# Kernel tuning notes

Measured on AMD Instinct MI355X. Metric: run time of the kernel, lower is better.

Reference implementation:

```python
import jax, jax.numpy as jnp
import numpy as np

HIDDEN = 256
BATCH = 8
N_A = 2048
N_B = 2048


def setup_inputs() -> dict:
    key = jax.random.key(0)
    ks = jax.random.split(key, 9)
    s = 1.0 / np.sqrt(HIDDEN)  # torch Linear default init scale
    return {
        "A": jax.random.normal(ks[0], (BATCH, N_A, HIDDEN), dtype=jnp.float32),
        "B": jax.random.normal(ks[1], (BATCH, N_B, HIDDEN), dtype=jnp.float32),
        "mask_B": jax.random.randint(ks[2], (BATCH, N_B), 0, 2, dtype=jnp.int32),
        "Wq": jax.random.uniform(ks[3], (HIDDEN, HIDDEN), jnp.float32, -s, s),
        "bq": jax.random.uniform(ks[4], (HIDDEN,), jnp.float32, -s, s),
        "Wk": jax.random.uniform(ks[5], (HIDDEN, HIDDEN), jnp.float32, -s, s),
        "bk": jax.random.uniform(ks[6], (HIDDEN,), jnp.float32, -s, s),
        "Wv": jax.random.uniform(ks[7], (HIDDEN, HIDDEN), jnp.float32, -s, s),
        "bv": jax.random.uniform(ks[8], (HIDDEN,), jnp.float32, -s, s),
    }


def reference(A, B, mask_B, Wq, bq, Wk, bk, Wv, bv):
    # QKV projections (torch Linear: x @ W.T + b)
    Q = A @ Wq.T + bq          # [B, N_A, H]
    K = B @ Wk.T + bk          # [B, N_B, H]
    V = B @ Wv.T + bv          # [B, N_B, H]
    scale = 1.0 / jnp.sqrt(jnp.asarray(Q.shape[-1], Q.dtype))
    scores = jnp.einsum("bnh,bmh->bnm", Q, K) * scale  # [B, N_A, N_B]
    neg_inf = jnp.finfo(scores.dtype).min
    scores = jnp.where(mask_B[:, None, :] == 0, neg_inf, scores)
    attn = jax.nn.softmax(scores, axis=-1)
    out = jnp.einsum("bnm,bmh->bnh", attn, V)          # [B, N_A, H]
    return out
```

## Files before the change

### kernel.cpp

```cpp
#include <hip/hip_runtime.h>


typedef __attribute__((ext_vector_type(8))) __bf16 bf16x8;
typedef __attribute__((ext_vector_type(4))) __bf16 bf16x4;
typedef __attribute__((ext_vector_type(4))) float f32x4;

#if __has_builtin(__builtin_amdgcn_exp2f)
#define EXP2(x) __builtin_amdgcn_exp2f(x)
#else
#define EXP2(x) exp2f(x)
#endif

#define MFMA16(a, b, c) __builtin_amdgcn_mfma_f32_16x16x32_bf16((a), (b), (c), 0, 0, 0)

typedef const __attribute__((address_space(1))) char gas_char;
typedef __attribute__((address_space(3))) char las_char;

static __device__ __forceinline__ void gload16(const void* g, void* l) {
  __builtin_amdgcn_global_load_lds((gas_char*)g, (las_char*)l, 16, 0, 0);
}

static __device__ __forceinline__ bf16x8 pack8(f32x4 a, f32x4 b) {
  bf16x8 r;
  r[0] = (__bf16)a[0]; r[1] = (__bf16)a[1]; r[2] = (__bf16)a[2]; r[3] = (__bf16)a[3];
  r[4] = (__bf16)b[0]; r[5] = (__bf16)b[1]; r[6] = (__bf16)b[2]; r[7] = (__bf16)b[3];
  return r;
}

__global__ void mask_kernel(const int* __restrict__ mask, float* __restrict__ mb) {
  int i = blockIdx.x * 256 + threadIdx.x;
  if (i < 8 * 2048) mb[i] = (mask[i] != 0) ? 0.0f : -1.0e30f;
}

__global__ __launch_bounds__(256, 4) void proj_kernel(
    const float* __restrict__ A, const float* __restrict__ Bm,
    const float* __restrict__ Wq, const float* __restrict__ bq,
    const float* __restrict__ Wk, const float* __restrict__ bk,
    const float* __restrict__ Wv, const float* __restrict__ bv,
    __bf16* __restrict__ QF, __bf16* __restrict__ KF, __bf16* __restrict__ VF) {
  __shared__ __bf16 Wl[256 * 64];
  const int pid = blockIdx.x;
  const int proj = pid >> 8;
  const int rb = (pid & 255) << 6;
  const float* __restrict__ X = (proj == 0) ? A : Bm;
  const float* __restrict__ W = (proj == 0) ? Wq : (proj == 1 ? Wk : Wv);
  const float* __restrict__ bias = (proj == 0) ? bq : (proj == 1 ? bk : bv);
  const int tid = threadIdx.x;
  const int w = tid >> 6, l = tid & 63, lo = l & 15, g = l >> 4;
  const int r0 = rb + w * 16;

  f32x4 acc[16];
#pragma unroll
  for (int j = 0; j < 16; ++j) acc[j] = (f32x4){0.f, 0.f, 0.f, 0.f};

  for (int qtr = 0; qtr < 4; ++qtr) {
    if (qtr) __syncthreads();
    for (int c = tid; c < 2048; c += 256) {
      int n = c >> 3;
      int k8 = (c & 7) << 3;
      const float* wp = &W[n * 256 + qtr * 64 + k8];
      f32x4 w0 = *(const f32x4*)wp;
      f32x4 w1 = *(const f32x4*)(wp + 4);
      int kx = k8 ^ ((n & 7) << 3);
      *(bf16x8*)&Wl[n * 64 + kx] = pack8(w0, w1);
    }
    __syncthreads();
#pragma unroll
    for (int ks2 = 0; ks2 < 2; ++ks2) {
      const int kg = qtr * 64 + ks2 * 32 + g * 8;
      const float* xp = &X[(r0 + lo) * 256 + kg];
      bf16x8 xf = pack8(*(const f32x4*)xp, *(const f32x4*)(xp + 4));
#pragma unroll
      for (int nt = 0; nt < 16; ++nt) {
        int n = nt * 16 + lo;
        int kchunk = (ks2 * 4 + g) ^ (n & 7);
        bf16x8 wf = *(const bf16x8*)&Wl[n * 64 + kchunk * 8];
        if (proj == 2) {
          acc[nt] = MFMA16(wf, xf, acc[nt]);
        } else {
          acc[nt] = MFMA16(xf, wf, acc[nt]);
        }
      }
    }
  }

  if (proj != 2) {
    const float cs = (proj == 0) ? 0.090168440f : 1.0f;
    __bf16* __restrict__ O = (proj == 0) ? QF : KF;
    const size_t rgbase = (size_t)(r0 >> 4) << 12;
#pragma unroll
    for (int nt = 0; nt < 16; ++nt) {
      int h = nt * 16 + lo;
      float bb = bias[h];
      size_t hpart = (size_t)((h >> 5) << 9) + (((h >> 3) & 3) << 7) + (h & 7);
#pragma unroll
      for (int r = 0; r < 4; ++r) {
        int R = r0 + g * 4 + r;
        O[rgbase + hpart + ((R & 15) << 3)] = (__bf16)((acc[nt][r] + bb) * cs);
      }
    }
  } else {
    const int bidx = r0 >> 11;
    const int nb = r0 & 2047;
    __bf16* __restrict__ Vo = VF + (size_t)bidx * 524288;
#pragma unroll
    for (int ht = 0; ht < 16; ++ht)
#pragma unroll
      for (int r = 0; r < 4; ++r) {
        int h = ht * 16 + g * 4 + r;
        int n = nb + lo;
        Vo[((size_t)(n >> 6) << 14) + ((h >> 4) << 10) + (((n >> 3) & 7) << 7) +
           ((h & 15) << 3) + (n & 7)] = (__bf16)(acc[ht][r] + bias[h]);
      }
  }
}

__global__ __launch_bounds__(256, 2) void attn_kernel(
    const __bf16* __restrict__ QF, const __bf16* __restrict__ KF,
    const __bf16* __restrict__ VF, const float* __restrict__ mb,
    __bf16* __restrict__ Opart, float* __restrict__ mpart,
    float* __restrict__ lpart, float* __restrict__ out,
    int chunk, int direct) {
  extern __shared__ char smem[];
  const int bid = blockIdx.x;
  const int b = bid & 7;
  const int rest = bid >> 3;
  const int qt = rest & 15;
  const int s = rest >> 4;
  const int tid = threadIdx.x;
  const int w = tid >> 6, l = tid & 63, lo = l & 15, g = l >> 4;
  const int q0 = qt * 128 + w * 32;
  const __bf16* __restrict__ Qb = QF + ((size_t)b * 2048 + q0) * 256;
  const __bf16* __restrict__ Kb = KF + (size_t)b * 2048 * 256;
  const __bf16* __restrict__ Vb = VF + (size_t)b * 524288;
  const float* __restrict__ mbb = mb + b * 2048;
  __bf16* Pw = (__bf16*)(smem + 65536) + w * 1280;
  float* mbl = (float*)(smem + 75776);

  bf16x8 qf[2][8];
#pragma unroll
  for (int u = 0; u < 2; ++u)
#pragma unroll
    for (int hs = 0; hs < 8; ++hs)
      qf[u][hs] = *(const bf16x8*)&Qb[u * 4096 + hs * 512 + l * 8];

  f32x4 oacc[2][16];
#pragma unroll
  for (int u = 0; u < 2; ++u)
#pragma unroll
    for (int i = 0; i < 16; ++i) oacc[u][i] = (f32x4){0.f, 0.f, 0.f, 0.f};
  float m[2] = {-3.0e28f, -3.0e28f}, lsum[2] = {0.f, 0.f};

  const int kv0 = s * chunk;
  const int niter = chunk >> 5;

  #define STAGE_K(kvb, buf)                                                   \
    {                                                                         \
      const char* gk = (const char*)(Kb + (size_t)(kvb) * 256) + w * 4096 +   \
                       l * 16;                                                \
      char* lk = smem + (buf)*16384 + w * 4096;                               \
      gload16(gk, lk);                                                        \
      gload16(gk + 1024, lk + 1024);                                          \
      gload16(gk + 2048, lk + 2048);                                          \
      gload16(gk + 3072, lk + 3072);                                          \
    }
  #define STAGE_V(kvb, buf)                                                   \
    {                                                                         \
      const char* gv = (const char*)(Vb + (((size_t)(kvb) >> 6) << 14) +      \
                                     (((kvb) >> 5) & 1) * 512) +              \
                       w * 8192 + l * 16;                                     \
      char* lv = smem + 32768 + (buf)*16384 + w * 4096;                       \
      gload16(gv, lv);                                                        \
      gload16(gv + 2048, lv + 1024);                                          \
      gload16(gv + 4096, lv + 2048);                                          \
      gload16(gv + 6144, lv + 3072);                                          \
    }

  if (!direct)
    for (int j = tid; j < chunk; j += 256) mbl[j] = mbb[kv0 + j];
  STAGE_K(kv0, 0);
  STAGE_V(kv0, 0);
  __syncthreads();

  for (int it = 0; it < niter; ++it) {
    const int kvb = kv0 + (it << 5);
    const int cur = it & 1;
    const bool pre = (it + 1 < niter);
    if (pre) STAGE_K(kvb + 32, cur ^ 1);
    const char* kbase = smem + cur * 16384;
    const char* vbase = smem + 32768 + cur * 16384;

    f32x4 sacc[2][2];
#pragma unroll
    for (int u = 0; u < 2; ++u)
#pragma unroll
      for (int t = 0; t < 2; ++t) sacc[u][t] = (f32x4){0.f, 0.f, 0.f, 0.f};
    __builtin_amdgcn_s_setprio(1);
#pragma unroll
    for (int t = 0; t < 2; ++t)
#pragma unroll
      for (int hs = 0; hs < 8; ++hs) {
        bf16x8 kf = *(const bf16x8*)(kbase + t * 8192 + hs * 1024 + l * 16);
        sacc[0][t] = MFMA16(kf, qf[0][hs], sacc[0][t]);
        sacc[1][t] = MFMA16(kf, qf[1][hs], sacc[1][t]);
      }
    __builtin_amdgcn_s_setprio(0);

    f32x4 bias4[2];
#pragma unroll
    for (int t = 0; t < 2; ++t) {
      if (direct)
        bias4[t] = *(const f32x4*)&mbb[kvb + t * 16 + g * 4];
      else
        bias4[t] = *(const f32x4*)&mbl[(it << 5) + t * 16 + g * 4];
    }
#pragma unroll
    for (int u = 0; u < 2; ++u) {
      float tmax = -3.4e38f;
#pragma unroll
      for (int t = 0; t < 2; ++t)
#pragma unroll
        for (int r = 0; r < 4; ++r) {
          sacc[u][t][r] += bias4[t][r];
          tmax = fmaxf(tmax, sacc[u][t][r]);
        }
      tmax = fmaxf(tmax, __shfl_xor(tmax, 16));
      tmax = fmaxf(tmax, __shfl_xor(tmax, 32));
      if (!__all(tmax <= m[u] + 8.0f)) {
        float mn = fmaxf(m[u], tmax);
        float f = EXP2(m[u] - mn);
        lsum[u] *= f;
#pragma unroll
        for (int i = 0; i < 16; ++i) {
          oacc[u][i][0] *= f; oacc[u][i][1] *= f;
          oacc[u][i][2] *= f; oacc[u][i][3] *= f;
        }
        m[u] = mn;
      }
#pragma unroll
      for (int t = 0; t < 2; ++t) {
        float p0 = EXP2(sacc[u][t][0] - m[u]);
        float p1 = EXP2(sacc[u][t][1] - m[u]);
        float p2 = EXP2(sacc[u][t][2] - m[u]);
        float p3 = EXP2(sacc[u][t][3] - m[u]);
        lsum[u] += (p0 + p1) + (p2 + p3);
        bf16x4 pk;
        pk[0] = (__bf16)p0; pk[1] = (__bf16)p1;
        pk[2] = (__bf16)p2; pk[3] = (__bf16)p3;
        *(bf16x4*)&Pw[u * 640 + lo * 40 + t * 16 + g * 4] = pk;
      }
    }
    bf16x8 pf[2];
#pragma unroll
    for (int u = 0; u < 2; ++u)
      pf[u] = *(const bf16x8*)&Pw[u * 640 + lo * 40 + g * 8];

    if (direct || !pre) {
      asm volatile("s_waitcnt vmcnt(0)" ::: "memory");
    } else {
      asm volatile("s_waitcnt vmcnt(4)" ::: "memory");
    }
    __builtin_amdgcn_s_barrier();
    __builtin_amdgcn_sched_barrier(0);

    if (pre) STAGE_V(kvb + 32, cur ^ 1);

    __builtin_amdgcn_s_setprio(1);
#pragma unroll
    for (int ht = 0; ht < 16; ++ht) {
      bf16x8 vf = *(const bf16x8*)(vbase + ht * 1024 + l * 16);
      oacc[0][ht] = MFMA16(vf, pf[0], oacc[0][ht]);
      oacc[1][ht] = MFMA16(vf, pf[1], oacc[1][ht]);
    }
    __builtin_amdgcn_s_setprio(0);

    if (direct || !pre) {
      asm volatile("s_waitcnt vmcnt(0)" ::: "memory");
    } else {
      asm volatile("s_waitcnt vmcnt(4)" ::: "memory");
    }
    __builtin_amdgcn_s_barrier();
    __builtin_amdgcn_sched_barrier(0);
  }

#pragma unroll
  for (int u = 0; u < 2; ++u) {
    float ls = lsum[u];
    ls += __shfl_xor(ls, 16);
    ls += __shfl_xor(ls, 32);
    const int q0u = q0 + u * 16;
    if (direct) {
      float inv = 1.0f / ls;
      float* __restrict__ Ob = out + ((size_t)b * 2048 + q0u) * 256;
#pragma unroll
      for (int ht = 0; ht < 16; ++ht) {
        f32x4 v = oacc[u][ht];
        v[0] *= inv; v[1] *= inv; v[2] *= inv; v[3] *= inv;
        *(f32x4*)&Ob[lo * 256 + ht * 16 + g * 4] = v;
      }
    } else {
      const size_t rowbase = (size_t)(s * 8 + b) * 2048 + q0u;
      __bf16* __restrict__ Ob = Opart + rowbase * 256;
#pragma unroll
      for (int ht = 0; ht < 16; ++ht) {
        f32x4 v = oacc[u][ht];
        bf16x4 pk;
        pk[0] = (__bf16)v[0]; pk[1] = (__bf16)v[1];
        pk[2] = (__bf16)v[2]; pk[3] = (__bf16)v[3];
        *(bf16x4*)&Ob[lo * 256 + ht * 16 + g * 4] = pk;
      }
      if (l < 16) {
        mpart[rowbase + lo] = m[u];
        lpart[rowbase + lo] = ls;
      }
    }
  }
}

__global__ __launch_bounds__(256) void combine_kernel(
    const __bf16* __restrict__ Opart, const float* __restrict__ mpart,
    const float* __restrict__ lpart, float* __restrict__ out, int nsplit) {
  int t = blockIdx.x * 256 + threadIdx.x;
  int row = t >> 6;
  int h4 = (t & 63) << 2;
  float M = -3.4e38f;
  for (int s = 0; s < nsplit; ++s) M = fmaxf(M, mpart[s * 16384 + row]);
  f32x4 acc = (f32x4){0.f, 0.f, 0.f, 0.f};
  float denom = 0.f;
  for (int s = 0; s < nsplit; ++s) {
    float wgt = EXP2(mpart[s * 16384 + row] - M);
    denom += wgt * lpart[s * 16384 + row];
    bf16x4 o = *(const bf16x4*)&Opart[((size_t)s * 16384 + row) * 256 + h4];
    acc[0] += wgt * (float)o[0]; acc[1] += wgt * (float)o[1];
    acc[2] += wgt * (float)o[2]; acc[3] += wgt * (float)o[3];
  }
  float inv = 1.0f / denom;
  f32x4 r;
  r[0] = acc[0] * inv; r[1] = acc[1] * inv;
  r[2] = acc[2] * inv; r[3] = acc[3] * inv;
  *(f32x4*)&out[(size_t)row * 256 + h4] = r;
}

extern "C" void kernel_launch(void* const* d_in, const int* in_sizes, int n_in,
                              void* d_out, int out_size, void* d_ws, size_t ws_size,
                              hipStream_t stream) {
  const float* A = (const float*)d_in[0];
  const float* B = (const float*)d_in[1];
  const int* mask = (const int*)d_in[2];
  const float* Wq = (const float*)d_in[3];
  const float* bq = (const float*)d_in[4];
  const float* Wk = (const float*)d_in[5];
  const float* bk = (const float*)d_in[6];
  const float* Wv = (const float*)d_in[7];
  const float* bv = (const float*)d_in[8];

  char* ws = (char*)d_ws;
  __bf16* QF = (__bf16*)(ws);
  __bf16* KF = (__bf16*)(ws + (8ull << 20));
  __bf16* VF = (__bf16*)(ws + (16ull << 20));
  float* mb = (float*)(ws + (24ull << 20));
  float* mpart = (float*)(ws + (24ull << 20) + 0x10000);
  float* lpart = (float*)(ws + (24ull << 20) + 0x60000);
  __bf16* Opart = (__bf16*)(ws + (25ull << 20));

  const size_t base = 25ull << 20;
  const size_t part = 8ull << 20;
  int S;
  if (ws_size >= base + 4 * part) S = 4;
  else if (ws_size >= base + 2 * part) S = 2;
  else if (ws_size >= base + 1 * part) S = 1;
  else S = 0;

  const int SMEM = 65536 + 4 * 1280 * 2 + 2048;
  (void)hipFuncSetAttribute((const void*)attn_kernel,
                            hipFuncAttributeMaxDynamicSharedMemorySize, SMEM);

  mask_kernel<<<64, 256, 0, stream>>>(mask, mb);
  proj_kernel<<<768, 256, 0, stream>>>(A, B, Wq, bq, Wk, bk, Wv, bv, QF, KF, VF);
  if (S == 0) {
    attn_kernel<<<128, 256, SMEM, stream>>>(QF, KF, VF, mb, nullptr, nullptr,
                                            nullptr, (float*)d_out, 2048, 1);
  } else {
    attn_kernel<<<128 * S, 256, SMEM, stream>>>(QF, KF, VF, mb, Opart, mpart,
                                                lpart, nullptr, 2048 / S, 0);
    combine_kernel<<<4096, 256, 0, stream>>>(Opart, mpart, lpart,
                                             (float*)d_out, S);
  }
}
```

Measured before the change: 102.7 us.

## Pre-convert weights to swizzled bf16 once and double-buffer them via async LDS loads

A new prep kernel converts Wq/Wk/Wv to bf16 in the swizzled LDS layout, folds the Q scale into Wq, and also builds the mask bias, replacing the separate mask kernel. The projection kernel then stages each weight quarter with global_load_lds into a double-buffered 64KB dynamic LDS region and prefetches all X fragments into registers up front. This removes the per-block fp32 weight conversion that every one of 768 blocks repeated, and overlaps weight loads with MFMA work. The cost is lower occupancy (launch bounds 2, 64KB LDS per block) and higher register pressure.

```diff
diff --git a/kernel.cpp b/kernel.cpp
--- a/kernel.cpp
+++ b/kernel.cpp
@@ -27,61 +27,102 @@
   return r;
 }
 
-__global__ void mask_kernel(const int* __restrict__ mask, float* __restrict__ mb) {
-  int i = blockIdx.x * 256 + threadIdx.x;
-  if (i < 8 * 2048) mb[i] = (mask[i] != 0) ? 0.0f : -1.0e30f;
-}
-
-__global__ __launch_bounds__(256, 4) void proj_kernel(
+__global__ __launch_bounds__(256) void wprep_kernel(
+    const float* __restrict__ Wq, const float* __restrict__ Wk,
+    const float* __restrict__ Wv, const int* __restrict__ mask,
+    __bf16* __restrict__ Wb, float* __restrict__ mb) {
+  const int bid = blockIdx.x;
+  if (bid < 96) {
+    int c = bid * 256 + threadIdx.x;
+    int w_id = c >> 13;
+    int j = c & 8191;
+    const float* __restrict__ W = (w_id == 0) ? Wq : (w_id == 1 ? Wk : Wv);
+    int n = j >> 5;
+    int c5 = j & 31;
+    int qtr = c5 >> 3;
+    int k8 = (c5 & 7) << 3;
+    const float* wp = &W[n * 256 + qtr * 64 + k8];
+    f32x4 w0 = *(const f32x4*)wp;
+    f32x4 w1 = *(const f32x4*)(wp + 4);
+    if (w_id == 0) {
+      const float cs = 0.090168440f;
+      w0[0] *= cs; w0[1] *= cs; w0[2] *= cs; w0[3] *= cs;
+      w1[0] *= cs; w1[1] *= cs; w1[2] *= cs; w1[3] *= cs;
+    }
+    int kx = k8 ^ ((n & 7) << 3);
+    *(bf16x8*)&Wb[(size_t)w_id * 65536 + qtr * 16384 + n * 64 + kx] =
+        pack8(w0, w1);
+  } else {
+    int i = (bid - 96) * 256 + threadIdx.x;
+    if (i < 8 * 2048) mb[i] = (mask[i] != 0) ? 0.0f : -1.0e30f;
+  }
+}
+
+__global__ __launch_bounds__(256, 2) void proj_kernel(
     const float* __restrict__ A, const float* __restrict__ Bm,
-    const float* __restrict__ Wq, const float* __restrict__ bq,
-    const float* __restrict__ Wk, const float* __restrict__ bk,
-    const float* __restrict__ Wv, const float* __restrict__ bv,
+    const __bf16* __restrict__ Wb,
+    const float* __restrict__ bq, const float* __restrict__ bk,
+    const float* __restrict__ bv,
     __bf16* __restrict__ QF, __bf16* __restrict__ KF, __bf16* __restrict__ VF) {
-  __shared__ __bf16 Wl[256 * 64];
+  extern __shared__ char smem[];
   const int pid = blockIdx.x;
   const int proj = pid >> 8;
   const int rb = (pid & 255) << 6;
   const float* __restrict__ X = (proj == 0) ? A : Bm;
-  const float* __restrict__ W = (proj == 0) ? Wq : (proj == 1 ? Wk : Wv);
+  const char* __restrict__ Wbp = (const char*)(Wb + (size_t)proj * 65536);
   const float* __restrict__ bias = (proj == 0) ? bq : (proj == 1 ? bk : bv);
   const int tid = threadIdx.x;
   const int w = tid >> 6, l = tid & 63, lo = l & 15, g = l >> 4;
   const int r0 = rb + w * 16;
 
+  bf16x8 xf[8];
+#pragma unroll
+  for (int q8 = 0; q8 < 8; ++q8) {
+    const float* xp = &X[(r0 + lo) * 256 + q8 * 32 + g * 8];
+    xf[q8] = pack8(*(const f32x4*)xp, *(const f32x4*)(xp + 4));
+  }
+
   f32x4 acc[16];
 #pragma unroll
   for (int j = 0; j < 16; ++j) acc[j] = (f32x4){0.f, 0.f, 0.f, 0.f};
 
+  #define STAGEW(qtr, buf)                                                    \
+    {                                                                         \
+      const char* gw = Wbp + (qtr)*32768 + w * 1024 + l * 16;                 \
+      char* lw = smem + (buf)*32768 + w * 1024;                               \
+      gload16(gw, lw);                                                        \
+      gload16(gw + 4096, lw + 4096);                                          \
+      gload16(gw + 8192, lw + 8192);                                          \
+      gload16(gw + 12288, lw + 12288);                                        \
+      gload16(gw + 16384, lw + 16384);                                        \
+      gload16(gw + 20480, lw + 20480);                                        \
+      gload16(gw + 24576, lw + 24576);                                        \
+      gload16(gw + 28672, lw + 28672);                                        \
+    }
+
+  STAGEW(0, 0);
+  __syncthreads();
+
   for (int qtr = 0; qtr < 4; ++qtr) {
-    if (qtr) __syncthreads();
-    for (int c = tid; c < 2048; c += 256) {
-      int n = c >> 3;
-      int k8 = (c & 7) << 3;
-      const float* wp = &W[n * 256 + qtr * 64 + k8];
-      f32x4 w0 = *(const f32x4*)wp;
-      f32x4 w1 = *(const f32x4*)(wp + 4);
-      int kx = k8 ^ ((n & 7) << 3);
-      *(bf16x8*)&Wl[n * 64 + kx] = pack8(w0, w1);
-    }
-    __syncthreads();
+    const int cur = qtr & 1;
+    if (qtr < 3) STAGEW(qtr + 1, cur ^ 1);
+    const __bf16* Wl = (const __bf16*)(smem + cur * 32768);
 #pragma unroll
     for (int ks2 = 0; ks2 < 2; ++ks2) {
-      const int kg = qtr * 64 + ks2 * 32 + g * 8;
-      const float* xp = &X[(r0 + lo) * 256 + kg];
-      bf16x8 xf = pack8(*(const f32x4*)xp, *(const f32x4*)(xp + 4));
+      bf16x8 xcur = xf[qtr * 2 + ks2];
 #pragma unroll
       for (int nt = 0; nt < 16; ++nt) {
         int n = nt * 16 + lo;
         int kchunk = (ks2 * 4 + g) ^ (n & 7);
         bf16x8 wf = *(const bf16x8*)&Wl[n * 64 + kchunk * 8];
         if (proj == 2) {
-          acc[nt] = MFMA16(wf, xf, acc[nt]);
+          acc[nt] = MFMA16(wf, xcur, acc[nt]);
         } else {
-          acc[nt] = MFMA16(xf, wf, acc[nt]);
+          acc[nt] = MFMA16(xcur, wf, acc[nt]);
         }
       }
     }
+    __syncthreads();
   }
 
   if (proj != 2) {
@@ -91,12 +132,12 @@
 #pragma unroll
     for (int nt = 0; nt < 16; ++nt) {
       int h = nt * 16 + lo;
-      float bb = bias[h];
+      float bb = bias[h] * cs;
       size_t hpart = (size_t)((h >> 5) << 9) + (((h >> 3) & 3) << 7) + (h & 7);
 #pragma unroll
       for (int r = 0; r < 4; ++r) {
         int R = r0 + g * 4 + r;
-        O[rgbase + hpart + ((R & 15) << 3)] = (__bf16)((acc[nt][r] + bb) * cs);
+        O[rgbase + hpart + ((R & 15) << 3)] = (__bf16)(acc[nt][r] + bb);
       }
     }
   } else {
@@ -361,6 +402,7 @@
   float* mb = (float*)(ws + (24ull << 20));
   float* mpart = (float*)(ws + (24ull << 20) + 0x10000);
   float* lpart = (float*)(ws + (24ull << 20) + 0x60000);
+  __bf16* Wb = (__bf16*)(ws + (24ull << 20) + 0xA0000);
   __bf16* Opart = (__bf16*)(ws + (25ull << 20));
 
   const size_t base = 25ull << 20;
@@ -371,12 +413,15 @@
   else if (ws_size >= base + 1 * part) S = 1;
   else S = 0;
 
+  const int PSMEM = 65536;
+  (void)hipFuncSetAttribute((const void*)proj_kernel,
+                            hipFuncAttributeMaxDynamicSharedMemorySize, PSMEM);
   const int SMEM = 65536 + 4 * 1280 * 2 + 2048;
   (void)hipFuncSetAttribute((const void*)attn_kernel,
                             hipFuncAttributeMaxDynamicSharedMemorySize, SMEM);
 
-  mask_kernel<<<64, 256, 0, stream>>>(mask, mb);
-  proj_kernel<<<768, 256, 0, stream>>>(A, B, Wq, bq, Wk, bk, Wv, bv, QF, KF, VF);
+  wprep_kernel<<<160, 256, 0, stream>>>(Wq, Wk, Wv, mask, Wb, mb);
+  proj_kernel<<<768, 256, PSMEM, stream>>>(A, B, Wb, bq, bk, bv, QF, KF, VF);
   if (S == 0) {
     attn_kernel<<<128, 256, SMEM, stream>>>(QF, KF, VF, mb, nullptr, nullptr,
                                             nullptr, (float*)d_out, 2048, 1);
```

Result: faster. 93.17 us (-9.3%).
